# Optimization experiments

Hardware: AMD Instinct MI355X
Metric: run time of the kernel (lower is better)

Reference implementation:

```python
import jax, jax.numpy as jnp
import numpy as np

B, D, NH, NL, NP, DFF = 2, 256, 8, 4, 4, 1024
HD = D // NH
SHAPES = [(128, 128), (64, 64), (32, 32), (16, 16)]  # (H, W) per level
S = sum(h * w for h, w in SHAPES)  # 21760
EPS = 1e-5


def _layer_norm(x, g, b):
    m = jnp.mean(x, -1, keepdims=True)
    v = jnp.mean(jnp.square(x - m), -1, keepdims=True)
    return (x - m) * jax.lax.rsqrt(v + EPS) * g + b


def _bilinear(v, grid, Hl, Wl):
    # v: [B, Hl*Wl, NH, HD]; grid: [B, S, NH, NP, 2] in [0,1] (x,y)
    # grid_sample semantics, align_corners=False, zero padding
    x = grid[..., 0] * Wl - 0.5
    y = grid[..., 1] * Hl - 0.5
    x0 = jnp.floor(x); y0 = jnp.floor(y)
    dx = x - x0; dy = y - y0
    x0i = x0.astype(jnp.int32); y0i = y0.astype(jnp.int32)

    def corner(xi, yi, w):
        valid = (xi >= 0) & (xi < Wl) & (yi >= 0) & (yi < Hl)
        idx = jnp.clip(yi, 0, Hl - 1) * Wl + jnp.clip(xi, 0, Wl - 1)  # [B,S,NH,NP]
        g_hw = lambda vb, ib: vb[ib]  # [HW,HD],[S,NP] -> [S,NP,HD]
        gat = jax.vmap(jax.vmap(g_hw, in_axes=(1, 1), out_axes=1))(v, idx)  # [B,S,NH,NP,HD]
        return gat * (w * valid.astype(v.dtype))[..., None]

    return (corner(x0i, y0i, (1 - dx) * (1 - dy))
            + corner(x0i + 1, y0i, dx * (1 - dy))
            + corner(x0i, y0i + 1, (1 - dx) * dy)
            + corner(x0i + 1, y0i + 1, dx * dy))


def _ms_deform_attn(query, value_in, ref_pts, shapes,
                    W_off, b_off, W_attn, b_attn, W_val, b_val, W_out, b_out):
    Bq, Sq = query.shape[:2]
    value = (value_in @ W_val + b_val).reshape(Bq, Sq, NH, HD)
    off = (query @ W_off + b_off).reshape(Bq, Sq, NH, NL, NP, 2)
    aw = (query @ W_attn + b_attn).reshape(Bq, Sq, NH, NL * NP)
    aw = jax.nn.softmax(aw, axis=-1).reshape(Bq, Sq, NH, NL, NP)
    # offset normalizer is (W, H) per level
    norm = jnp.array([[w, h] for h, w in shapes], dtype=query.dtype)
    loc = ref_pts[:, :, None, :, None, :] + off / norm[None, None, None, :, None, :]
    out = jnp.zeros((Bq, Sq, NH, HD), query.dtype)
    start = 0
    for l, (Hl, Wl) in enumerate(shapes):
        v_l = value[:, start:start + Hl * Wl]
        sampled = _bilinear(v_l, loc[:, :, :, l], Hl, Wl)  # [B,S,NH,NP,HD]
        out = out + jnp.einsum('bqhp,bqhpd->bqhd', aw[:, :, :, l], sampled)
        start += Hl * Wl
    return out.reshape(Bq, Sq, D) @ W_out + b_out


def setup_inputs() -> dict:
    key = jax.random.key(0)
    ks = jax.random.split(key, 16)
    sc = 0.02
    lsi = np.cumsum([0] + [h * w for h, w in SHAPES[:-1]])
    return dict(
        src=jax.random.normal(ks[0], (B, S, D), jnp.float32),
        pos=jax.random.normal(ks[1], (B, S, D), jnp.float32),
        reference_points=jax.random.uniform(ks[2], (B, S, NL, 2), jnp.float32),
        spatial_shapes=jnp.array(SHAPES, jnp.int32),
        level_start_index=jnp.array(lsi, jnp.int32),
        W_off=sc * jax.random.normal(ks[3], (D, NH * NL * NP * 2), jnp.float32),
        b_off=jnp.zeros((NH * NL * NP * 2,), jnp.float32),
        W_attn=sc * jax.random.normal(ks[4], (D, NH * NL * NP), jnp.float32),
        b_attn=jnp.zeros((NH * NL * NP,), jnp.float32),
        W_val=sc * jax.random.normal(ks[5], (D, D), jnp.float32),
        b_val=jnp.zeros((D,), jnp.float32),
        W_out=sc * jax.random.normal(ks[6], (D, D), jnp.float32),
        b_out=jnp.zeros((D,), jnp.float32),
        g1=jnp.ones((D,), jnp.float32), be1=jnp.zeros((D,), jnp.float32),
        W_ff1=sc * jax.random.normal(ks[7], (D, DFF), jnp.float32),
        b_ff1=jnp.zeros((DFF,), jnp.float32),
        W_ff2=sc * jax.random.normal(ks[8], (DFF, D), jnp.float32),
        b_ff2=jnp.zeros((D,), jnp.float32),
        g2=jnp.ones((D,), jnp.float32), be2=jnp.zeros((D,), jnp.float32),
    )


def reference(src, pos, reference_points, spatial_shapes, level_start_index,
              W_off, b_off, W_attn, b_attn, W_val, b_val, W_out, b_out,
              g1, be1, W_ff1, b_ff1, W_ff2, b_ff2, g2, be2):
    # spatial_shapes is static metadata (defines per-level reshapes)
    shapes = [tuple(int(v) for v in row) for row in np.asarray(spatial_shapes)]
    attn = _ms_deform_attn(src + pos, src, reference_points, shapes,
                           W_off, b_off, W_attn, b_attn, W_val, b_val, W_out, b_out)
    x = _layer_norm(src + attn, g1, be1)
    ffn = jax.nn.relu(x @ W_ff1 + b_ff1) @ W_ff2 + b_ff2
    return _layer_norm(x + ffn, g2, be2)
```

## Files before the change

kernel.cpp:

```cpp
#include <hip/hip_runtime.h>
#include <cstdint>
#include <cstddef>

#define B_   2
#define S_   21760
#define M_   (B_ * S_)
#define D_   256
#define DFF_ 1024
#define EPS_ 1e-5f

typedef __attribute__((ext_vector_type(8))) short short8;
typedef __attribute__((ext_vector_type(4))) float f32x4;
typedef __attribute__((ext_vector_type(2))) float f32x2;

__device__ __forceinline__ ushort f2bf(float f) {
    uint x = __float_as_uint(f);
    return (ushort)((x + 0x7fffu + ((x >> 16) & 1u)) >> 16);
}
__device__ __forceinline__ float bf2f(ushort u) {
    return __uint_as_float(((uint)u) << 16);
}

#define CVT_BLOCKS 10880
__global__ __launch_bounds__(256) void prep_all(
    const float* __restrict__ src, const float* __restrict__ pos,
    ushort* __restrict__ sb, ushort* __restrict__ qb,
    const float* __restrict__ Wval, const float* __restrict__ Woff,
    const float* __restrict__ Wattn, const float* __restrict__ Wout,
    const float* __restrict__ Wff1, const float* __restrict__ Wff2,
    const float* __restrict__ boff, const float* __restrict__ battn,
    ushort* __restrict__ WT, float* __restrict__ bias_oa)
{
    if (blockIdx.x < CVT_BLOCKS) {
        const size_t i = ((size_t)blockIdx.x * 256 + threadIdx.x) * 4;
        const float4 s = *(const float4*)(src + i);
        const float4 p = *(const float4*)(pos + i);
        ushort4 so, qo;
        so.x = f2bf(s.x); so.y = f2bf(s.y); so.z = f2bf(s.z); so.w = f2bf(s.w);
        qo.x = f2bf(s.x + p.x); qo.y = f2bf(s.y + p.y);
        qo.z = f2bf(s.z + p.z); qo.w = f2bf(s.w + p.w);
        *(ushort4*)(sb + i) = so;
        *(ushort4*)(qb + i) = qo;
        return;
    }
    const int i = (blockIdx.x - CVT_BLOCKS) * 256 + threadIdx.x;
    if (i < 65536) {
        const int n = i >> 8, k = i & 255;
        WT[i] = f2bf(Wval[(size_t)k * 256 + n]);
    } else if (i < 163840) {
        const int j = i - 65536;
        const int n = j >> 8, k = j & 255;
        WT[i] = (n < 256) ? f2bf(Woff[(size_t)k * 256 + n])
                          : f2bf(Wattn[(size_t)k * 128 + (n - 256)]);
    } else if (i < 229376) {
        const int j = i - 163840;
        const int n = j >> 8, k = j & 255;
        WT[i] = f2bf(Wout[(size_t)k * 256 + n]);
    } else if (i < 491520) {
        const int j = i - 229376;
        const int n = j >> 8, k = j & 255;
        WT[i] = f2bf(Wff1[(size_t)k * 1024 + n]);
    } else if (i < 753664) {
        const int j = i - 491520;
        const int n = j >> 10, k = j & 1023;
        WT[i] = f2bf(Wff2[(size_t)k * 256 + n]);
    } else if (i < 753664 + 384) {
        const int j = i - 753664;
        bias_oa[j] = (j < 256) ? boff[j] : battn[j - 256];
    }
}

__global__ __launch_bounds__(256) void mgemm(
    const ushort* __restrict__ A, const ushort* __restrict__ WT,
    const float* __restrict__ bias, ushort* __restrict__ C,
    int M, int N, int K, int relu, int mode)
{
    __shared__ __align__(16) ushort Als[128 * 32];
    __shared__ __align__(16) ushort Bls[128 * 32];

    const int nwg = gridDim.x;
    const int bid = blockIdx.x;
    const int q8 = nwg >> 3, r8 = nwg & 7;
    const int xcd = bid & 7, blk = bid >> 3;
    const int wg = (xcd < r8 ? xcd * (q8 + 1) : r8 * (q8 + 1) + (xcd - r8) * q8) + blk;
    const int gx = N >> 7;
    const int n0 = (wg % gx) << 7;
    const int m0 = (wg / gx) << 7;

    const int tid = threadIdx.x;
    const int wv = tid >> 6, ln = tid & 63;
    const int wm = wv >> 1, wn = wv & 1;

    const int lrow = ln >> 2, lcol = (ln & 3) * 8;

    f32x4 acc[4][4];
    const f32x4 zz = {0.f, 0.f, 0.f, 0.f};
    #pragma unroll
    for (int i = 0; i < 4; i++)
        #pragma unroll
        for (int j = 0; j < 4; j++) acc[i][j] = zz;

    for (int k0 = 0; k0 < K; k0 += 32) {
        __syncthreads();
        #pragma unroll
        for (int r = 0; r < 2; ++r) {
            const int c = r * 4 + wv;
            const ushort* ga = A + (size_t)(m0 + c * 16 + lrow) * K + k0 + lcol;
            __builtin_amdgcn_global_load_lds(
                (const __attribute__((address_space(1))) uint*)ga,
                (__attribute__((address_space(3))) uint*)(Als + c * 512), 16, 0, 0);
            const ushort* gb = WT + (size_t)(n0 + c * 16 + lrow) * K + k0 + lcol;
            __builtin_amdgcn_global_load_lds(
                (const __attribute__((address_space(1))) uint*)gb,
                (__attribute__((address_space(3))) uint*)(Bls + c * 512), 16, 0, 0);
        }
        __syncthreads();

        const int fr = ln & 15, kb = (ln >> 4) * 8;
        short8 af[4], bfr[4];
        #pragma unroll
        for (int i = 0; i < 4; i++)
            af[i] = *(const short8*)&Als[(wm * 64 + i * 16 + fr) * 32 + kb];
        #pragma unroll
        for (int j = 0; j < 4; j++)
            bfr[j] = *(const short8*)&Bls[(wn * 64 + j * 16 + fr) * 32 + kb];
        #pragma unroll
        for (int i = 0; i < 4; i++)
            #pragma unroll
            for (int j = 0; j < 4; j++)
                acc[i][j] = __builtin_amdgcn_mfma_f32_16x16x32_bf16(
                    af[i], bfr[j], acc[i][j], 0, 0, 0);
    }

    uint8_t* C8 = (uint8_t*)C;
    const int fr = ln & 15, rq = (ln >> 4) * 4;
    #pragma unroll
    for (int j = 0; j < 4; j++) {
        const int col = n0 + wn * 64 + j * 16 + fr;
        const float bv = bias[col];
        #pragma unroll
        for (int i = 0; i < 4; i++) {
            #pragma unroll
            for (int r = 0; r < 4; r++) {
                const int row = m0 + wm * 64 + i * 16 + rq + r;
                float v = acc[i][j][r] + bv;
                if (relu) v = fmaxf(v, 0.f);
                if (mode == 0) {
                    C[(size_t)row * N + col] = f2bf(v);
                } else {
                    const int bb = (row >= S_) ? 1 : 0;
                    const int loc = row - bb * S_;
                    const int hh = col >> 5, ch = col & 31;
                    const int pk = __builtin_amdgcn_cvt_pk_fp8_f32(v, v, 0, false);
                    C8[((size_t)(bb * 8 + hh) * S_ + loc) * 32 + ch] = (uint8_t)(pk & 0xff);
                }
            }
        }
    }
}

__global__ __launch_bounds__(256) void ln_row(
    const ushort* __restrict__ a16, const ushort* __restrict__ r16,
    const float* __restrict__ g, const float* __restrict__ be,
    float* __restrict__ o32, ushort* __restrict__ o16)
{
    const int wv = threadIdx.x >> 6, ln = threadIdx.x & 63;
    const int row = blockIdx.x * 4 + wv;
    const int col = ln * 4;
    const size_t base = (size_t)row * 256 + col;

    const ushort4 av = *(const ushort4*)(a16 + base);
    const ushort4 rv = *(const ushort4*)(r16 + base);
    float v0 = bf2f(av.x) + bf2f(rv.x);
    float v1 = bf2f(av.y) + bf2f(rv.y);
    float v2 = bf2f(av.z) + bf2f(rv.z);
    float v3 = bf2f(av.w) + bf2f(rv.w);

    float s = v0 + v1 + v2 + v3;
    float s2 = v0 * v0 + v1 * v1 + v2 * v2 + v3 * v3;
    #pragma unroll
    for (int o = 32; o > 0; o >>= 1) {
        s  += __shfl_down(s, o);
        s2 += __shfl_down(s2, o);
    }
    s = __shfl(s, 0);
    s2 = __shfl(s2, 0);
    const float mean = s * (1.f / 256.f);
    const float var = s2 * (1.f / 256.f) - mean * mean;
    const float rstd = rsqrtf(var + EPS_);

    const float4 gv = *(const float4*)(g + col);
    const float4 bv = *(const float4*)(be + col);
    const float o0 = (v0 - mean) * rstd * gv.x + bv.x;
    const float o1 = (v1 - mean) * rstd * gv.y + bv.y;
    const float o2 = (v2 - mean) * rstd * gv.z + bv.z;
    const float o3 = (v3 - mean) * rstd * gv.w + bv.w;

    if (o32) {
        float4 o; o.x = o0; o.y = o1; o.z = o2; o.w = o3;
        *(float4*)(o32 + base) = o;
    } else {
        ushort4 o; o.x = f2bf(o0); o.y = f2bf(o1); o.z = f2bf(o2); o.w = f2bf(o3);
        *(ushort4*)(o16 + base) = o;
    }
}

__global__ __launch_bounds__(256) void sample6(
    const uint8_t* __restrict__ value, const ushort* __restrict__ offaw,
    const float* __restrict__ refp, ushort* __restrict__ samp)
{
    const int nwg = M_ / 8;
    const int bid = blockIdx.x;
    const int wg = (bid & 7) * (nwg >> 3) + (bid >> 3);

    const int t = threadIdx.x;
    const int q = wg * 8 + (t >> 5);
    const int w = t & 31;
    const int h = w >> 2, cg = w & 3;
    const int half = cg >> 1;
    const int b = q / S_;

    const ushort* awq = offaw + (size_t)q * 384 + 256 + h * 16;
    const uint4 la = *(const uint4*)awq;
    const uint4 lb = *(const uint4*)(awq + 8);
    const uint lgu[8] = {la.x, la.y, la.z, la.w, lb.x, lb.y, lb.z, lb.w};
    float aj[16];
    float mx = -1e30f;
    #pragma unroll
    for (int k = 0; k < 8; k++) {
        aj[2 * k]     = bf2f((ushort)(lgu[k] & 0xffff));
        aj[2 * k + 1] = bf2f((ushort)(lgu[k] >> 16));
        mx = fmaxf(mx, fmaxf(aj[2 * k], aj[2 * k + 1]));
    }
    float sum = 0.f;
    #pragma unroll
    for (int s = 0; s < 16; s++) { aj[s] = __expf(aj[s] - mx); sum += aj[s]; }
    const float inv = 1.f / sum;
    #pragma unroll
    for (int s = 0; s < 16; s++) aj[s] *= inv;

    const ushort* ofq = offaw + (size_t)q * 384 + h * 32;
    const uint4 o0 = *(const uint4*)ofq;
    const uint4 o1 = *(const uint4*)(ofq + 8);
    const uint4 o2 = *(const uint4*)(ofq + 16);
    const uint4 o3 = *(const uint4*)(ofq + 24);
    const uint ou[16] = {o0.x, o0.y, o0.z, o0.w, o1.x, o1.y, o1.z, o1.w,
                         o2.x, o2.y, o2.z, o2.w, o3.x, o3.y, o3.z, o3.w};
    const float* rp = refp + (size_t)q * 8;
    const float4 rpa = *(const float4*)rp;
    const float4 rpb = *(const float4*)(rp + 4);
    const float rxa[4] = {rpa.x, rpa.z, rpb.x, rpb.z};
    const float rya[4] = {rpa.y, rpa.w, rpb.y, rpb.w};
    const int   stv[4] = {0, 16384, 20480, 21504};

    const uint8_t* vb = value + (size_t)(b * 8 + h) * S_ * 32 + cg * 16;

    f32x2 acc[8];
    #pragma unroll
    for (int k = 0; k < 8; k++) acc[k] = (f32x2){0.f, 0.f};

    #pragma unroll
    for (int l = 0; l < 4; l++) {
        const int Wl = 128 >> l;
        const float fW = (float)Wl;
        const int st = stv[l];
        const float rx = rxa[l], ry = rya[l];

        float rw[8];
        int   rix[8];
        #pragma unroll
        for (int j = 0; j < 4; j++) {
            const int s = l * 4 + j;
            const float ox = bf2f((ushort)(ou[s] & 0xffff));
            const float oy = bf2f((ushort)(ou[s] >> 16));
            const float x = fmaf(rx, fW, ox) - 0.5f;
            const float y = fmaf(ry, fW, oy) - 0.5f;
            const float fx0 = floorf(x), fy0 = floorf(y);
            const float dx = x - fx0, dy = y - fy0;
            const int x0 = (int)fx0, y0 = (int)fy0;

            const int bx = min(max(x0, 0), Wl - 2);
            const float mwx0 = ((x0 >= 0) & (x0 < Wl)) ? (1.f - dx) : 0.f;
            const float mwx1 = ((x0 + 1 >= 0) & (x0 + 1 < Wl)) ? dx : 0.f;
            const int xc0 = min(max(x0, 0), Wl - 1);
            const int xc1 = min(max(x0 + 1, 0), Wl - 1);
            const float wAx = (xc0 == bx ? mwx0 : 0.f) + (xc1 == bx ? mwx1 : 0.f);
            const float wBx = (xc0 == bx + 1 ? mwx0 : 0.f) + (xc1 == bx + 1 ? mwx1 : 0.f);
            const float wsel = half ? wBx : wAx;

            const int yc0 = min(max(y0, 0), Wl - 1);
            const int yc1 = min(max(y0 + 1, 0), Wl - 1);
            const float mwy0 = ((y0 >= 0) & (y0 < Wl)) ? (1.f - dy) : 0.f;
            const float mwy1 = ((y0 + 1 >= 0) & (y0 + 1 < Wl)) ? dy : 0.f;

            const float aw = aj[s] * wsel;
            rw[2 * j]      = aw * mwy0;
            rix[2 * j]     = (st + yc0 * Wl + bx) * 32;
            rw[2 * j + 1]  = aw * mwy1;
            rix[2 * j + 1] = (st + yc1 * Wl + bx) * 32;
        }

        #pragma unroll
        for (int r = 0; r < 8; r++) {
            const uint4 u = *(const uint4*)(vb + rix[r]);
            const f32x2 w2 = {rw[r], rw[r]};
            acc[0] += w2 * __builtin_amdgcn_cvt_pk_f32_fp8((int)u.x, false);
            acc[1] += w2 * __builtin_amdgcn_cvt_pk_f32_fp8((int)u.x, true);
            acc[2] += w2 * __builtin_amdgcn_cvt_pk_f32_fp8((int)u.y, false);
            acc[3] += w2 * __builtin_amdgcn_cvt_pk_f32_fp8((int)u.y, true);
            acc[4] += w2 * __builtin_amdgcn_cvt_pk_f32_fp8((int)u.z, false);
            acc[5] += w2 * __builtin_amdgcn_cvt_pk_f32_fp8((int)u.z, true);
            acc[6] += w2 * __builtin_amdgcn_cvt_pk_f32_fp8((int)u.w, false);
            acc[7] += w2 * __builtin_amdgcn_cvt_pk_f32_fp8((int)u.w, true);
        }
    }

    #pragma unroll
    for (int k = 0; k < 8; k++) {
        acc[k].x += __shfl_xor(acc[k].x, 2);
        acc[k].y += __shfl_xor(acc[k].y, 2);
    }

    f32x2 r0, r1, r2, r3;
    if (half == 0) { r0 = acc[0]; r1 = acc[1]; r2 = acc[2]; r3 = acc[3]; }
    else           { r0 = acc[4]; r1 = acc[5]; r2 = acc[6]; r3 = acc[7]; }

    const int ch_start = (cg & 1) * 16 + half * 8;
    uint4 o;
    o.x = (uint)f2bf(r0.x) | ((uint)f2bf(r0.y) << 16);
    o.y = (uint)f2bf(r1.x) | ((uint)f2bf(r1.y) << 16);
    o.z = (uint)f2bf(r2.x) | ((uint)f2bf(r2.y) << 16);
    o.w = (uint)f2bf(r3.x) | ((uint)f2bf(r3.y) << 16);
    *(uint4*)(samp + (size_t)q * 256 + h * 32 + ch_start) = o;
}

extern "C" void kernel_launch(void* const* d_in, const int* in_sizes, int n_in,
                              void* d_out, int out_size, void* d_ws, size_t ws_size,
                              hipStream_t stream)
{
    const float* src    = (const float*)d_in[0];
    const float* pos    = (const float*)d_in[1];
    const float* refp   = (const float*)d_in[2];
    const float* W_off  = (const float*)d_in[5];
    const float* b_off  = (const float*)d_in[6];
    const float* W_attn = (const float*)d_in[7];
    const float* b_attn = (const float*)d_in[8];
    const float* W_val  = (const float*)d_in[9];
    const float* b_val  = (const float*)d_in[10];
    const float* W_out  = (const float*)d_in[11];
    const float* b_out  = (const float*)d_in[12];
    const float* g1     = (const float*)d_in[13];
    const float* be1    = (const float*)d_in[14];
    const float* W_ff1  = (const float*)d_in[15];
    const float* b_ff1  = (const float*)d_in[16];
    const float* W_ff2  = (const float*)d_in[17];
    const float* b_ff2  = (const float*)d_in[18];
    const float* g2     = (const float*)d_in[19];
    const float* be2    = (const float*)d_in[20];
    float* out = (float*)d_out;

    const size_t szMDh = (size_t)M_ * 256 * 2;
    const size_t szOAh = (size_t)M_ * 384 * 2;

    char* ws = (char*)d_ws;
    ushort* WT      = (ushort*)ws;
    ushort* WT_val  = WT;
    ushort* WT_oa   = WT + 65536;
    ushort* WT_out  = WT + 163840;
    ushort* WT_ff1  = WT + 229376;
    ushort* WT_ff2  = WT + 491520;
    float*  bias_oa = (float*)(ws + 1507328);

    const size_t o_src  = 2097152;
    const size_t o_q    = o_src + szMDh;
    const size_t o_val  = o_q   + szMDh;
    const size_t o_oa   = o_val + szMDh;
    const size_t o_x    = o_oa  + szOAh;
    const size_t o_ffn  = o_x   + szMDh;

    ushort* src_bf  = (ushort*)(ws + o_src);
    ushort* q_bf    = (ushort*)(ws + o_q);
    ushort* val_f8  = (ushort*)(ws + o_val);
    ushort* offaw   = (ushort*)(ws + o_oa);
    ushort* x_bf    = (ushort*)(ws + o_x);
    ushort* ffn_bf  = (ushort*)(ws + o_ffn);
    ushort* samp_bf = q_bf;
    ushort* attn_bf = val_f8;
    ushort* hbuf    = src_bf;

    prep_all<<<CVT_BLOCKS + 2947, 256, 0, stream>>>(
        src, pos, src_bf, q_bf,
        W_val, W_off, W_attn, W_out, W_ff1, W_ff2, b_off, b_attn, WT, bias_oa);
    mgemm<<<2 * (M_ / 128), 256, 0, stream>>>(src_bf, WT_val, b_val, val_f8, M_, 256, 256, 0, 2);
    mgemm<<<3 * (M_ / 128), 256, 0, stream>>>(q_bf, WT_oa, bias_oa, offaw, M_, 384, 256, 0, 0);
    sample6<<<M_ / 8, 256, 0, stream>>>((const uint8_t*)val_f8, offaw, refp, samp_bf);
    mgemm<<<2 * (M_ / 128), 256, 0, stream>>>(samp_bf, WT_out, b_out, attn_bf, M_, 256, 256, 0, 0);
    ln_row<<<M_ / 4, 256, 0, stream>>>(attn_bf, src_bf, g1, be1, nullptr, x_bf);
    mgemm<<<8 * (M_ / 128), 256, 0, stream>>>(x_bf, WT_ff1, b_ff1, hbuf, M_, DFF_, 256, 1, 0);
    mgemm<<<2 * (M_ / 128), 256, 0, stream>>>(hbuf, WT_ff2, b_ff2, ffn_bf, M_, 256, DFF_, 0, 0);
    ln_row<<<M_ / 4, 256, 0, stream>>>(ffn_bf, x_bf, g2, be2, out, nullptr);
}
```

Measured before the change: 274.6 us.

## Split sampling-coordinate math across lanes and broadcast via shuffles

Result: no change. 272.3 us (-0.8%).

```diff
diff --git a/kernel.cpp b/kernel.cpp
--- a/kernel.cpp
+++ b/kernel.cpp
@@ -205,7 +205,7 @@
     }
 }
 
-__global__ __launch_bounds__(256) void sample6(
+__global__ __launch_bounds__(256) void sample7(
     const uint8_t* __restrict__ value, const ushort* __restrict__ offaw,
     const float* __restrict__ refp, ushort* __restrict__ samp)
 {
@@ -219,91 +219,82 @@
     const int h = w >> 2, cg = w & 3;
     const int half = cg >> 1;
     const int b = q / S_;
-
-    const ushort* awq = offaw + (size_t)q * 384 + 256 + h * 16;
-    const uint4 la = *(const uint4*)awq;
-    const uint4 lb = *(const uint4*)(awq + 8);
-    const uint lgu[8] = {la.x, la.y, la.z, la.w, lb.x, lb.y, lb.z, lb.w};
-    float aj[16];
-    float mx = -1e30f;
-    #pragma unroll
-    for (int k = 0; k < 8; k++) {
-        aj[2 * k]     = bf2f((ushort)(lgu[k] & 0xffff));
-        aj[2 * k + 1] = bf2f((ushort)(lgu[k] >> 16));
-        mx = fmaxf(mx, fmaxf(aj[2 * k], aj[2 * k + 1]));
-    }
-    float sum = 0.f;
-    #pragma unroll
-    for (int s = 0; s < 16; s++) { aj[s] = __expf(aj[s] - mx); sum += aj[s]; }
-    const float inv = 1.f / sum;
-    #pragma unroll
-    for (int s = 0; s < 16; s++) aj[s] *= inv;
-
-    const ushort* ofq = offaw + (size_t)q * 384 + h * 32;
-    const uint4 o0 = *(const uint4*)ofq;
-    const uint4 o1 = *(const uint4*)(ofq + 8);
-    const uint4 o2 = *(const uint4*)(ofq + 16);
-    const uint4 o3 = *(const uint4*)(ofq + 24);
-    const uint ou[16] = {o0.x, o0.y, o0.z, o0.w, o1.x, o1.y, o1.z, o1.w,
-                         o2.x, o2.y, o2.z, o2.w, o3.x, o3.y, o3.z, o3.w};
-    const float* rp = refp + (size_t)q * 8;
-    const float4 rpa = *(const float4*)rp;
-    const float4 rpb = *(const float4*)(rp + 4);
-    const float rxa[4] = {rpa.x, rpa.z, rpb.x, rpb.z};
-    const float rya[4] = {rpa.y, rpa.w, rpb.y, rpb.w};
-    const int   stv[4] = {0, 16384, 20480, 21504};
+    const int gbase = (t & 63) & ~3;
+
+    const int Wl = 128 >> cg;
+    const float fW = (float)Wl;
+    const int st = (cg == 0) ? 0 : (cg == 1) ? 16384 : (cg == 2) ? 20480 : 21504;
+
+    const ushort* awq = offaw + (size_t)q * 384 + 256 + h * 16 + cg * 4;
+    const uint2 lg = *(const uint2*)awq;
+    const float l0 = bf2f((ushort)(lg.x & 0xffff)), l1 = bf2f((ushort)(lg.x >> 16));
+    const float l2 = bf2f((ushort)(lg.y & 0xffff)), l3 = bf2f((ushort)(lg.y >> 16));
+    float mx = fmaxf(fmaxf(l0, l1), fmaxf(l2, l3));
+    mx = fmaxf(mx, __shfl_xor(mx, 1));
+    mx = fmaxf(mx, __shfl_xor(mx, 2));
+    const float e0 = __expf(l0 - mx), e1 = __expf(l1 - mx);
+    const float e2 = __expf(l2 - mx), e3 = __expf(l3 - mx);
+    float sm = e0 + e1 + e2 + e3;
+    sm += __shfl_xor(sm, 1);
+    sm += __shfl_xor(sm, 2);
+    const float inv = 1.f / sm;
+    const float aj[4] = {e0 * inv, e1 * inv, e2 * inv, e3 * inv};
+
+    const ushort* ofq = offaw + (size_t)q * 384 + h * 32 + cg * 8;
+    const uint4 of = *(const uint4*)ofq;
+    const uint ou[4] = {of.x, of.y, of.z, of.w};
+    const float rx = refp[(size_t)q * 8 + cg * 2];
+    const float ry = refp[(size_t)q * 8 + cg * 2 + 1];
+
+    int  rxo[8];
+    uint wpk[8];
+    #pragma unroll
+    for (int j = 0; j < 4; j++) {
+        const float ox = bf2f((ushort)(ou[j] & 0xffff));
+        const float oy = bf2f((ushort)(ou[j] >> 16));
+        const float x = fmaf(rx, fW, ox) - 0.5f;
+        const float y = fmaf(ry, fW, oy) - 0.5f;
+        const float fx0 = floorf(x), fy0 = floorf(y);
+        const float dx = x - fx0, dy = y - fy0;
+        const int x0 = (int)fx0, y0 = (int)fy0;
+
+        const int bx = min(max(x0, 0), Wl - 2);
+        const float mwx0 = ((x0 >= 0) & (x0 < Wl)) ? (1.f - dx) : 0.f;
+        const float mwx1 = ((x0 + 1 >= 0) & (x0 + 1 < Wl)) ? dx : 0.f;
+        const int xc0 = min(max(x0, 0), Wl - 1);
+        const int xc1 = min(max(x0 + 1, 0), Wl - 1);
+        const float wAx = (xc0 == bx ? mwx0 : 0.f) + (xc1 == bx ? mwx1 : 0.f);
+        const float wBx = (xc0 == bx + 1 ? mwx0 : 0.f) + (xc1 == bx + 1 ? mwx1 : 0.f);
+
+        const int yc0 = min(max(y0, 0), Wl - 1);
+        const int yc1 = min(max(y0 + 1, 0), Wl - 1);
+        const float mwy0 = ((y0 >= 0) & (y0 < Wl)) ? (1.f - dy) : 0.f;
+        const float mwy1 = ((y0 + 1 >= 0) & (y0 + 1 < Wl)) ? dy : 0.f;
+
+        const float a = aj[j];
+        const float wA0 = a * wAx * mwy0, wB0 = a * wBx * mwy0;
+        const float wA1 = a * wAx * mwy1, wB1 = a * wBx * mwy1;
+        rxo[2 * j]     = (st + yc0 * Wl + bx) * 32;
+        rxo[2 * j + 1] = (st + yc1 * Wl + bx) * 32;
+        wpk[2 * j]     = (uint)f2bf(wA0) | ((uint)f2bf(wB0) << 16);
+        wpk[2 * j + 1] = (uint)f2bf(wA1) | ((uint)f2bf(wB1) << 16);
+    }
 
     const uint8_t* vb = value + (size_t)(b * 8 + h) * S_ * 32 + cg * 16;
-
     f32x2 acc[8];
     #pragma unroll
     for (int k = 0; k < 8; k++) acc[k] = (f32x2){0.f, 0.f};
 
     #pragma unroll
-    for (int l = 0; l < 4; l++) {
-        const int Wl = 128 >> l;
-        const float fW = (float)Wl;
-        const int st = stv[l];
-        const float rx = rxa[l], ry = rya[l];
-
-        float rw[8];
-        int   rix[8];
-        #pragma unroll
-        for (int j = 0; j < 4; j++) {
-            const int s = l * 4 + j;
-            const float ox = bf2f((ushort)(ou[s] & 0xffff));
-            const float oy = bf2f((ushort)(ou[s] >> 16));
-            const float x = fmaf(rx, fW, ox) - 0.5f;
-            const float y = fmaf(ry, fW, oy) - 0.5f;
-            const float fx0 = floorf(x), fy0 = floorf(y);
-            const float dx = x - fx0, dy = y - fy0;
-            const int x0 = (int)fx0, y0 = (int)fy0;
-
-            const int bx = min(max(x0, 0), Wl - 2);
-            const float mwx0 = ((x0 >= 0) & (x0 < Wl)) ? (1.f - dx) : 0.f;
-            const float mwx1 = ((x0 + 1 >= 0) & (x0 + 1 < Wl)) ? dx : 0.f;
-            const int xc0 = min(max(x0, 0), Wl - 1);
-            const int xc1 = min(max(x0 + 1, 0), Wl - 1);
-            const float wAx = (xc0 == bx ? mwx0 : 0.f) + (xc1 == bx ? mwx1 : 0.f);
-            const float wBx = (xc0 == bx + 1 ? mwx0 : 0.f) + (xc1 == bx + 1 ? mwx1 : 0.f);
-            const float wsel = half ? wBx : wAx;
-
-            const int yc0 = min(max(y0, 0), Wl - 1);
-            const int yc1 = min(max(y0 + 1, 0), Wl - 1);
-            const float mwy0 = ((y0 >= 0) & (y0 < Wl)) ? (1.f - dy) : 0.f;
-            const float mwy1 = ((y0 + 1 >= 0) & (y0 + 1 < Wl)) ? dy : 0.f;
-
-            const float aw = aj[s] * wsel;
-            rw[2 * j]      = aw * mwy0;
-            rix[2 * j]     = (st + yc0 * Wl + bx) * 32;
-            rw[2 * j + 1]  = aw * mwy1;
-            rix[2 * j + 1] = (st + yc1 * Wl + bx) * 32;
-        }
-
+    for (int ol = 0; ol < 4; ol++) {
+        const int srcl = gbase + ol;
         #pragma unroll
         for (int r = 0; r < 8; r++) {
-            const uint4 u = *(const uint4*)(vb + rix[r]);
-            const f32x2 w2 = {rw[r], rw[r]};
+            const int  rix = __shfl(rxo[r], srcl, 64);
+            const uint wp  = (uint)__shfl((int)wpk[r], srcl, 64);
+            const float wv = bf2f((ushort)(half ? (wp >> 16) : (wp & 0xffffu)));
+            const uint4 u = *(const uint4*)(vb + rix);
+            const f32x2 w2 = {wv, wv};
             acc[0] += w2 * __builtin_amdgcn_cvt_pk_f32_fp8((int)u.x, false);
             acc[1] += w2 * __builtin_amdgcn_cvt_pk_f32_fp8((int)u.x, true);
             acc[2] += w2 * __builtin_amdgcn_cvt_pk_f32_fp8((int)u.y, false);
@@ -393,7 +384,7 @@
         W_val, W_off, W_attn, W_out, W_ff1, W_ff2, b_off, b_attn, WT, bias_oa);
     mgemm<<<2 * (M_ / 128), 256, 0, stream>>>(src_bf, WT_val, b_val, val_f8, M_, 256, 256, 0, 2);
     mgemm<<<3 * (M_ / 128), 256, 0, stream>>>(q_bf, WT_oa, bias_oa, offaw, M_, 384, 256, 0, 0);
-    sample6<<<M_ / 8, 256, 0, stream>>>((const uint8_t*)val_f8, offaw, refp, samp_bf);
+    sample7<<<M_ / 8, 256, 0, stream>>>((const uint8_t*)val_f8, offaw, refp, samp_bf);
     mgemm<<<2 * (M_ / 128), 256, 0, stream>>>(samp_bf, WT_out, b_out, attn_bf, M_, 256, 256, 0, 0);
     ln_row<<<M_ / 4, 256, 0, stream>>>(attn_bf, src_bf, g1, be1, nullptr, x_bf);
     mgemm<<<8 * (M_ / 128), 256, 0, stream>>>(x_bf, WT_ff1, b_ff1, hbuf, M_, DFF_, 256, 1, 0);
```
